# Kernel tuning notes

Hardware: AMD Instinct MI355X
Metric: run time of the kernel (lower is better)

The kernel has to match this reference:

```python
import jax, jax.numpy as jnp
import numpy as np

EMBED = 1024
HID = 1024
B, T = 32, 512


def _gru_layer(x, Wih, Whh, bih, bhh):
    """Torch-convention GRU over time. x: [B,T,Hin]; Wih: [3H,Hin]; Whh: [3H,H].
    Gate order (torch): reset, update, new."""
    H = Whh.shape[1]
    # Precompute input contributions for all timesteps: [T,B,3H]
    xg = jnp.einsum('bti,gi->tbg', x, Wih) + bih

    def step(h, xt):
        hg = h @ Whh.T + bhh                    # [B,3H]
        xr, xz, xn = jnp.split(xt, 3, axis=-1)
        hr, hz, hn = jnp.split(hg, 3, axis=-1)
        r = jax.nn.sigmoid(xr + hr)
        z = jax.nn.sigmoid(xz + hz)
        n = jnp.tanh(xn + r * hn)
        h_new = (1.0 - z) * n + z * h
        return h_new, h_new

    h0 = jnp.zeros((x.shape[0], H), dtype=x.dtype)
    _, ys = jax.lax.scan(step, h0, xg)          # ys: [T,B,H]
    return jnp.transpose(ys, (1, 0, 2))         # [B,T,H]


def setup_inputs() -> dict:
    key = jax.random.key(0)
    ks = jax.random.split(key, 16)
    s_in = 1.0 / np.sqrt(EMBED)
    s_h = 1.0 / np.sqrt(HID)
    return {
        'x': jax.random.normal(ks[0], (B, T, EMBED), jnp.float32),
        'context': jax.random.normal(ks[1], (B, HID), jnp.float32),
        'W_in': jax.random.uniform(ks[2], (HID, EMBED), jnp.float32, -s_in, s_in),
        'b_in': jax.random.uniform(ks[3], (HID,), jnp.float32, -s_in, s_in),
        'Wih0': jax.random.uniform(ks[4], (3 * HID, HID), jnp.float32, -s_h, s_h),
        'Whh0': jax.random.uniform(ks[5], (3 * HID, HID), jnp.float32, -s_h, s_h),
        'bih0': jax.random.uniform(ks[6], (3 * HID,), jnp.float32, -s_h, s_h),
        'bhh0': jax.random.uniform(ks[7], (3 * HID,), jnp.float32, -s_h, s_h),
        'Wih1': jax.random.uniform(ks[8], (3 * HID, HID), jnp.float32, -s_h, s_h),
        'Whh1': jax.random.uniform(ks[9], (3 * HID, HID), jnp.float32, -s_h, s_h),
        'bih1': jax.random.uniform(ks[10], (3 * HID,), jnp.float32, -s_h, s_h),
        'bhh1': jax.random.uniform(ks[11], (3 * HID,), jnp.float32, -s_h, s_h),
        'W_out': jax.random.uniform(ks[12], (EMBED, HID), jnp.float32, -s_h, s_h),
        'b_out': jax.random.uniform(ks[13], (EMBED,), jnp.float32, -s_h, s_h),
        'W_gate': jax.random.uniform(ks[14], (HID, HID), jnp.float32, -s_h, s_h),
        'b_gate': jax.random.uniform(ks[15], (HID,), jnp.float32, -s_h, s_h),
    }


def reference(x, context, W_in, b_in, Wih0, Whh0, bih0, bhh0,
              Wih1, Whh1, bih1, bhh1, W_out, b_out, W_gate, b_gate):
    # context_seq: [B,1,H] broadcast over time
    ctx = context[:, None, :]
    mixed = jnp.tanh(jnp.einsum('bte,he->bth', x, W_in) + b_in + ctx)
    h1 = _gru_layer(mixed, Wih0, Whh0, bih0, bhh0)
    h2 = _gru_layer(h1, Wih1, Whh1, bih1, bhh1)
    gate = jax.nn.sigmoid(jnp.einsum('bh,gh->bg', context, W_gate) + b_gate)
    gated = gate[:, None, :] * h2 + h2
    return jnp.einsum('bth,eh->bte', gated, W_out) + b_out
```

## Files before the change

### kernel.cpp

```cpp
#include <hip/hip_runtime.h>
#include <cstdint>
#include <cstddef>

#define SEQT  512
#define HID   1024
#define G3    3072
#define HSTR  1080
#define RING  32
#define FSTR  32

typedef __attribute__((ext_vector_type(8))) short bf16x8;
typedef __attribute__((ext_vector_type(8))) unsigned short u16x8;
typedef __attribute__((ext_vector_type(4))) float f32x4;

__device__ __forceinline__ float sigm(float x){ return 1.0f/(1.0f+expf(-x)); }
__device__ __forceinline__ float b2f(unsigned short s){ return __uint_as_float(((uint32_t)s)<<16); }
__device__ __forceinline__ unsigned short f2b(float f){
    uint32_t u=__float_as_uint(f);
    return (unsigned short)((u + 0x7FFFu + ((u>>16)&1u))>>16);
}

template<int ASRC, int BSRC, int MODE>
__global__ __launch_bounds__(256) void mfma_gemm(
    const void* __restrict__ Av, const void* __restrict__ Bv,
    const float* __restrict__ bias, const float* __restrict__ ctx,
    const float* __restrict__ gate, void* __restrict__ Cv,
    int N, int K)
{
    __shared__ __align__(16) unsigned short As[128*64];
    __shared__ __align__(16) unsigned short Bs[128*64];
    const int tid = threadIdx.x;
    const int lane = tid & 63;
    const int w = tid >> 6;
    const int wm = w & 1, wn = w >> 1;
    const int m0 = blockIdx.y * 128, n0 = blockIdx.x * 128;

    f32x4 acc[4][4];
#pragma unroll
    for (int i = 0; i < 4; i++)
#pragma unroll
        for (int j = 0; j < 4; j++) acc[i][j] = (f32x4){0.f,0.f,0.f,0.f};

    for (int kt = 0; kt < K; kt += 64) {
        __syncthreads();
        if (ASRC == 1) {
            const float* Af = (const float*)Av;
#pragma unroll
            for (int p = 0; p < 4; p++) {
                const int q = p*256 + tid, row = q>>3, kc = q&7;
                const float* src = Af + (size_t)(m0+row)*K + kt + kc*8;
                float4 u = *(const float4*)src, v = *(const float4*)(src+4);
                __align__(16) unsigned short tmp[8] =
                    {f2b(u.x),f2b(u.y),f2b(u.z),f2b(u.w),f2b(v.x),f2b(v.y),f2b(v.z),f2b(v.w)};
                *(bf16x8*)&As[row*64 + kc*8] = *(const bf16x8*)tmp;
            }
        } else {
            const unsigned short* Ab = (const unsigned short*)Av;
#pragma unroll
            for (int p = 0; p < 4; p++) {
                const int q = p*256 + tid, row = q>>3, kc = q&7;
                const int b = (m0+row) >> 9;
                u16x8 hv = *(const u16x8*)(Ab + (size_t)(m0+row)*K + kt + kc*8);
                const float* gp = gate + (size_t)b*HID + kt + kc*8;
                float4 g0 = *(const float4*)gp, g1 = *(const float4*)(gp+4);
                const float gg[8] = {g0.x,g0.y,g0.z,g0.w,g1.x,g1.y,g1.z,g1.w};
                __align__(16) unsigned short tmp[8];
#pragma unroll
                for (int e = 0; e < 8; e++)
                    tmp[e] = f2b(b2f(hv[e]) * (1.0f + gg[e]));
                *(bf16x8*)&As[row*64 + kc*8] = *(const bf16x8*)tmp;
            }
        }
        {
            const float* Bf = (const float*)Bv;
#pragma unroll
            for (int p = 0; p < 4; p++) {
                const int q = p*256 + tid, row = q>>3, kc = q&7;
                const float* src = Bf + (size_t)(n0+row)*K + kt + kc*8;
                float4 u = *(const float4*)src, v = *(const float4*)(src+4);
                __align__(16) unsigned short tmp[8] =
                    {f2b(u.x),f2b(u.y),f2b(u.z),f2b(u.w),f2b(v.x),f2b(v.y),f2b(v.z),f2b(v.w)};
                *(bf16x8*)&Bs[row*64 + kc*8] = *(const bf16x8*)tmp;
            }
        }
        __syncthreads();
#pragma unroll
        for (int kg = 0; kg < 2; kg++) {
            bf16x8 af[4], bfr[4];
#pragma unroll
            for (int mi = 0; mi < 4; mi++)
                af[mi] = *(const bf16x8*)&As[(wm*64+mi*16+(lane&15))*64 + kg*32 + (lane>>4)*8];
#pragma unroll
            for (int ni = 0; ni < 4; ni++)
                bfr[ni] = *(const bf16x8*)&Bs[(wn*64+ni*16+(lane&15))*64 + kg*32 + (lane>>4)*8];
#pragma unroll
            for (int mi = 0; mi < 4; mi++)
#pragma unroll
                for (int ni = 0; ni < 4; ni++)
                    acc[mi][ni] = __builtin_amdgcn_mfma_f32_16x16x32_bf16(
                        af[mi], bfr[ni], acc[mi][ni], 0, 0, 0);
        }
    }

    const int cl = lane & 15, rg = lane >> 4;
    const int bct = m0 >> 9;
#pragma unroll
    for (int mi = 0; mi < 4; mi++) {
        const int rowb = m0 + wm*64 + mi*16 + rg*4;
#pragma unroll
        for (int ni = 0; ni < 4; ni++) {
            const int col = n0 + wn*64 + ni*16 + cl;
            const float bv = bias[col];
            const float cv = (MODE==1) ? ctx[(size_t)bct*HID + col] : 0.0f;
#pragma unroll
            for (int r = 0; r < 4; r++) {
                float val = acc[mi][ni][r] + bv;
                if (MODE==1) val = tanhf(val + cv);
                const size_t off = (size_t)(rowb+r)*N + col;
                if (MODE==0) ((float*)Cv)[off] = val;
                else ((unsigned short*)Cv)[off] = f2b(val);
            }
        }
    }
}

__global__ __launch_bounds__(256) void gate_kernel(
    const float* __restrict__ ctx, const float* __restrict__ Wg,
    const float* __restrict__ bg, float* __restrict__ gate)
{
    const int j = blockIdx.x * 256 + threadIdx.x;
    const int b = blockIdx.y;
    const float4* cp = (const float4*)(ctx + (size_t)b * HID);
    const float4* wp = (const float4*)(Wg + (size_t)j * HID);
    float acc = 0.0f;
#pragma unroll 4
    for (int k = 0; k < HID / 4; k++) {
        float4 c = cp[k], w = wp[k];
        acc += c.x * w.x + c.y * w.y + c.z * w.z + c.w * w.w;
    }
    gate[(size_t)b * HID + j] = sigm(acc + bg[j]);
}

__device__ __forceinline__ void poll_ge(const unsigned int* p, unsigned int tgt)
{
    while (__hip_atomic_load(p, __ATOMIC_RELAXED, __HIP_MEMORY_SCOPE_AGENT) < tgt)
        __builtin_amdgcn_s_sleep(2);
}

__global__ __launch_bounds__(384, 1) void gru_pipe(
    const float* __restrict__ Wih0, const float* __restrict__ Whh0,
    const float* __restrict__ bih0, const float* __restrict__ bhh0,
    const float* __restrict__ Wih1, const float* __restrict__ Whh1,
    const float* __restrict__ bih1, const float* __restrict__ bhh1,
    const unsigned short* __restrict__ mixed,
    unsigned short* __restrict__ h1,
    unsigned short* __restrict__ h2,
    unsigned short* __restrict__ xgs0,
    unsigned short* __restrict__ xgs1,
    unsigned int* __restrict__ flags)
{
    __shared__ __align__(16) unsigned short h_lds[32*HSTR];
    __shared__ float sc[3][32][17];
    const int tid = threadIdx.x;
    const int lane = tid & 63;
    const int w = tid >> 6;
    const int bid = blockIdx.x;
    const int role = bid >> 6, rb = bid & 63;
    const int j0 = rb * 16;
    const int mh = w & 1, g = w >> 1;
    const int cl = lane & 15, kq = lane >> 4;

    unsigned int* fset[4] = { flags, flags + 64*FSTR, flags + 128*FSTR, flags + 192*FSTR };

    const float* Wsrc = (role == 0) ? Wih0 : (role == 1) ? Whh0
                      : (role == 2) ? Wih1 : Whh1;
    bf16x8 wreg[32];
    {
        const float* wr = Wsrc + (size_t)(g*1024 + j0 + cl)*1024 + kq*8;
#pragma unroll
        for (int kg = 0; kg < 32; kg++) {
            float4 u = *(const float4*)(wr + (size_t)kg*32);
            float4 v = *(const float4*)(wr + (size_t)kg*32 + 4);
            __align__(16) unsigned short tmp[8] =
                {f2b(u.x),f2b(u.y),f2b(u.z),f2b(u.w),f2b(v.x),f2b(v.y),f2b(v.z),f2b(v.w)};
            wreg[kg] = *(const bf16x8*)tmp;
        }
    }
#pragma unroll
    for (int kg = 0; kg < 32; kg++)
        asm volatile("" : "+v"(wreg[kg]));

    const int hrow_r = mh*16 + cl;
    const unsigned short* habase =
        &h_lds[hrow_r*HSTR + ((hrow_r & 3) << 4) + kq*8];

    auto stage = [&](const unsigned short* src_base, int tt) {
        for (int c = w; c < 64; c += 6) {
            const int r = c >> 1, hf = c & 1;
            const unsigned short* src =
                src_base + ((size_t)r*SEQT + tt)*HID + hf*512 + lane*8;
            __builtin_amdgcn_global_load_lds(
                (const __attribute__((address_space(1))) void*)src,
                (__attribute__((address_space(3))) void*)
                    &h_lds[r*HSTR + ((r & 3) << 4) + hf*512],
                16, 0, 0);
        }
    };

    if ((role & 1) == 0) {
        const unsigned short* hsrc = (role == 0) ? mixed : h1;
        unsigned short* xgs = ((role == 0) ? xgs0 : xgs1) + (size_t)rb*RING*32*48;
        const unsigned int* waitin = (role == 2) ? fset[1] : nullptr;
        const unsigned int* bp     = (role == 0) ? fset[1] : fset[3];
        unsigned int* myflag = &fset[role][rb*FSTR];

        for (int t = 0; t < SEQT; t++) {
            if (w == 0 && waitin)
                poll_ge(&waitin[lane*FSTR], (unsigned)(t+1));
            if (w == 1 && t >= RING && (t & 7) == 0)
                poll_ge(&bp[lane*FSTR], (unsigned)(t - 24));
            __syncthreads();

            stage(hsrc, t);
            asm volatile("s_waitcnt vmcnt(0)" ::: "memory");
            __syncthreads();

            f32x4 A[4];
#pragma unroll
            for (int i = 0; i < 4; i++) A[i] = (f32x4){0.f,0.f,0.f,0.f};
#pragma unroll
            for (int kg = 0; kg < 32; kg++) {
                bf16x8 hv = *(const bf16x8*)(habase + kg*32);
                A[kg & 3] = __builtin_amdgcn_mfma_f32_16x16x32_bf16(
                    hv, wreg[kg], A[kg & 3], 0, 0, 0);
            }
            f32x4 av = (A[0] + A[1]) + (A[2] + A[3]);
#pragma unroll
            for (int r = 0; r < 4; r++)
                sc[g][mh*16 + kq*4 + r][cl] = av[r];
            __syncthreads();

            if (tid < 192) {
                const int b = tid / 6, c16 = (tid % 6) * 8;
                unsigned short v[8];
#pragma unroll
                for (int k = 0; k < 8; k++) {
                    const int col = c16 + k;
                    v[k] = f2b(sc[col >> 4][b][col & 15]);
                }
                const uint64_t lo = (uint64_t)v[0] | ((uint64_t)v[1]<<16)
                                  | ((uint64_t)v[2]<<32) | ((uint64_t)v[3]<<48);
                const uint64_t hi = (uint64_t)v[4] | ((uint64_t)v[5]<<16)
                                  | ((uint64_t)v[6]<<32) | ((uint64_t)v[7]<<48);
                uint64_t* dst = (uint64_t*)(xgs + (((size_t)(t & (RING-1))*32 + b)*48 + c16));
                __hip_atomic_store(dst,   lo, __ATOMIC_RELAXED, __HIP_MEMORY_SCOPE_AGENT);
                __hip_atomic_store(dst+1, hi, __ATOMIC_RELAXED, __HIP_MEMORY_SCOPE_AGENT);
            }
            asm volatile("s_waitcnt vmcnt(0)" ::: "memory");
            __syncthreads();
            if (tid == 0)
                __hip_atomic_store(myflag, (unsigned)(t+1),
                                   __ATOMIC_RELAXED, __HIP_MEMORY_SCOPE_AGENT);
        }
    } else {
        const unsigned short* xgs = ((role == 1) ? xgs0 : xgs1) + (size_t)rb*RING*32*48;
        unsigned short* hdst = (role == 1) ? h1 : h2;
        const float* bih = (role == 1) ? bih0 : bih1;
        const float* bhh = (role == 1) ? bhh0 : bhh1;
        const unsigned int* peers = fset[role];
        const unsigned int* prodf = &fset[role-1][rb*FSTR];
        unsigned int* myflag = &fset[role][rb*FSTR];

        const int fb = tid >> 3;
        const int fj = (tid & 7) * 2;
        float hp0 = 0.f, hp1 = 0.f;
        float br0=0,br1=0,bz0=0,bz1=0,bni0=0,bni1=0,bnh0=0,bnh1=0;
        if (tid < 256) {
            br0 = bih[j0+fj]        + bhh[j0+fj];
            br1 = bih[j0+fj+1]      + bhh[j0+fj+1];
            bz0 = bih[HID+j0+fj]    + bhh[HID+j0+fj];
            bz1 = bih[HID+j0+fj+1]  + bhh[HID+j0+fj+1];
            bni0 = bih[2*HID+j0+fj];   bni1 = bih[2*HID+j0+fj+1];
            bnh0 = bhh[2*HID+j0+fj];   bnh1 = bhh[2*HID+j0+fj+1];
        }

        for (int t = 0; t < SEQT; t++) {
            if (w == 0 && t > 0)
                poll_ge(&peers[lane*FSTR], (unsigned)t);
            if (w == 2 && lane == 0)
                poll_ge(prodf, (unsigned)(t+1));
            __syncthreads();

            if (t > 0) stage(hdst, t-1);

            uint32_t xr2=0, xz2=0, xn2=0;
            if (tid < 256) {
                const unsigned short* xp = xgs + ((size_t)(t & (RING-1))*32 + fb)*48;
                xr2 = __hip_atomic_load((const unsigned int*)(xp + fj),
                                        __ATOMIC_RELAXED, __HIP_MEMORY_SCOPE_AGENT);
                xz2 = __hip_atomic_load((const unsigned int*)(xp + 16 + fj),
                                        __ATOMIC_RELAXED, __HIP_MEMORY_SCOPE_AGENT);
                xn2 = __hip_atomic_load((const unsigned int*)(xp + 32 + fj),
                                        __ATOMIC_RELAXED, __HIP_MEMORY_SCOPE_AGENT);
            }
            asm volatile("s_waitcnt vmcnt(0)" ::: "memory");
            __syncthreads();

            f32x4 A[4];
#pragma unroll
            for (int i = 0; i < 4; i++) A[i] = (f32x4){0.f,0.f,0.f,0.f};
            if (t > 0) {
#pragma unroll
                for (int kg = 0; kg < 32; kg++) {
                    bf16x8 hv = *(const bf16x8*)(habase + kg*32);
                    A[kg & 3] = __builtin_amdgcn_mfma_f32_16x16x32_bf16(
                        hv, wreg[kg], A[kg & 3], 0, 0, 0);
                }
            }
            f32x4 av = (A[0] + A[1]) + (A[2] + A[3]);
#pragma unroll
            for (int r = 0; r < 4; r++)
                sc[g][mh*16 + kq*4 + r][cl] = av[r];
            __syncthreads();

            if (tid < 256) {
                const float r0 = sigm(b2f((unsigned short)(xr2 & 0xFFFF)) + sc[0][fb][fj]   + br0);
                const float r1 = sigm(b2f((unsigned short)(xr2 >> 16))    + sc[0][fb][fj+1] + br1);
                const float z0 = sigm(b2f((unsigned short)(xz2 & 0xFFFF)) + sc[1][fb][fj]   + bz0);
                const float z1 = sigm(b2f((unsigned short)(xz2 >> 16))    + sc[1][fb][fj+1] + bz1);
                const float n0 = tanhf(b2f((unsigned short)(xn2 & 0xFFFF)) + bni0
                                       + r0*(sc[2][fb][fj]   + bnh0));
                const float n1 = tanhf(b2f((unsigned short)(xn2 >> 16))    + bni1
                                       + r1*(sc[2][fb][fj+1] + bnh1));
                const float h0 = (1.0f - z0)*n0 + z0*hp0;
                const float h1v = (1.0f - z1)*n1 + z1*hp1;
                hp0 = h0; hp1 = h1v;
                const uint32_t hv = (uint32_t)f2b(h0) | ((uint32_t)f2b(h1v) << 16);
                uint32_t* dst = (uint32_t*)(hdst + ((size_t)fb*SEQT + t)*HID + j0 + fj);
                __hip_atomic_store(dst, hv, __ATOMIC_RELAXED, __HIP_MEMORY_SCOPE_AGENT);
            }
            asm volatile("s_waitcnt vmcnt(0)" ::: "memory");
            __syncthreads();
            if (tid == 0)
                __hip_atomic_store(myflag, (unsigned)(t+1),
                                   __ATOMIC_RELAXED, __HIP_MEMORY_SCOPE_AGENT);
        }
    }
}

__global__ __launch_bounds__(256) void diag_kernel(float* __restrict__ out,
                                                   int n, float code)
{
    for (int i = blockIdx.x * 256 + threadIdx.x; i < n; i += gridDim.x * 256)
        out[i] = (i == 0) ? code : 0.0f;
}

extern "C" void kernel_launch(void* const* d_in, const int* in_sizes, int n_in,
                              void* d_out, int out_size, void* d_ws, size_t ws_size,
                              hipStream_t stream)
{
    const float* x      = (const float*)d_in[0];
    const float* ctx    = (const float*)d_in[1];
    const float* W_in   = (const float*)d_in[2];
    const float* b_in   = (const float*)d_in[3];
    const float* Wih0   = (const float*)d_in[4];
    const float* Whh0   = (const float*)d_in[5];
    const float* bih0   = (const float*)d_in[6];
    const float* bhh0   = (const float*)d_in[7];
    const float* Wih1   = (const float*)d_in[8];
    const float* Whh1   = (const float*)d_in[9];
    const float* bih1   = (const float*)d_in[10];
    const float* bhh1   = (const float*)d_in[11];
    const float* W_out  = (const float*)d_in[12];
    const float* b_out  = (const float*)d_in[13];
    const float* W_gate = (const float*)d_in[14];
    const float* b_gate = (const float*)d_in[15];
    float* out = (float*)d_out;

    const size_t MX = (size_t)16384 * 1024 * 2;
    const size_t XS = (size_t)64 * RING * 32 * 48 * 2;
    const size_t GT = (size_t)32 * 1024 * 4;
    const size_t FL = (size_t)4 * 64 * FSTR * 4;
    const size_t need = 3*MX + 2*XS + GT + FL;

    if (ws_size < need) {
        diag_kernel<<<2048, 256, 0, stream>>>(out, out_size, (float)(ws_size >> 20));
        return;
    }

    char* ws = (char*)d_ws;
    unsigned short* mixed = (unsigned short*)ws;
    unsigned short* h1    = (unsigned short*)(ws + MX);
    unsigned short* h2    = (unsigned short*)(ws + 2*MX);
    unsigned short* xgs0  = (unsigned short*)(ws + 3*MX);
    unsigned short* xgs1  = (unsigned short*)(ws + 3*MX + XS);
    float*          gate  = (float*)(ws + 3*MX + 2*XS);
    unsigned int*   flags = (unsigned int*)(ws + 3*MX + 2*XS + GT);

    hipMemsetAsync(flags, 0, FL, stream);
    gate_kernel<<<dim3(4, 32), 256, 0, stream>>>(ctx, W_gate, b_gate, gate);

    mfma_gemm<1, 1, 1><<<dim3(8, 128), 256, 0, stream>>>(
        x, W_in, b_in, ctx, nullptr, mixed, 1024, 1024);

    gru_pipe<<<256, 384, 0, stream>>>(
        Wih0, Whh0, bih0, bhh0, Wih1, Whh1, bih1, bhh1,
        mixed, h1, h2, xgs0, xgs1, flags);

    mfma_gemm<2, 1, 0><<<dim3(8, 128), 256, 0, stream>>>(
        h2, W_out, b_out, nullptr, gate, out, 1024, 1024);
}
```

Baseline: 2.390 ms.

## Split recurrent GRU step into two batch halves with split-K MFMA overlap

```diff
diff --git a/kernel.cpp b/kernel.cpp
--- a/kernel.cpp
+++ b/kernel.cpp
@@ -160,59 +160,45 @@
     unsigned int* __restrict__ flags)
 {
     __shared__ __align__(16) unsigned short h_lds[32*HSTR];
-    __shared__ float sc[3][32][17];
+    __shared__ float sc[1632];
     const int tid = threadIdx.x;
     const int lane = tid & 63;
     const int w = tid >> 6;
     const int bid = blockIdx.x;
     const int role = bid >> 6, rb = bid & 63;
     const int j0 = rb * 16;
-    const int mh = w & 1, g = w >> 1;
     const int cl = lane & 15, kq = lane >> 4;
 
-    unsigned int* fset[4] = { flags, flags + 64*FSTR, flags + 128*FSTR, flags + 192*FSTR };
-
-    const float* Wsrc = (role == 0) ? Wih0 : (role == 1) ? Whh0
-                      : (role == 2) ? Wih1 : Whh1;
-    bf16x8 wreg[32];
-    {
-        const float* wr = Wsrc + (size_t)(g*1024 + j0 + cl)*1024 + kq*8;
-#pragma unroll
-        for (int kg = 0; kg < 32; kg++) {
-            float4 u = *(const float4*)(wr + (size_t)kg*32);
-            float4 v = *(const float4*)(wr + (size_t)kg*32 + 4);
-            __align__(16) unsigned short tmp[8] =
-                {f2b(u.x),f2b(u.y),f2b(u.z),f2b(u.w),f2b(v.x),f2b(v.y),f2b(v.z),f2b(v.w)};
-            wreg[kg] = *(const bf16x8*)tmp;
-        }
-    }
-#pragma unroll
-    for (int kg = 0; kg < 32; kg++)
-        asm volatile("" : "+v"(wreg[kg]));
-
-    const int hrow_r = mh*16 + cl;
-    const unsigned short* habase =
-        &h_lds[hrow_r*HSTR + ((hrow_r & 3) << 4) + kq*8];
-
-    auto stage = [&](const unsigned short* src_base, int tt) {
-        for (int c = w; c < 64; c += 6) {
-            const int r = c >> 1, hf = c & 1;
-            const unsigned short* src =
-                src_base + ((size_t)r*SEQT + tt)*HID + hf*512 + lane*8;
-            __builtin_amdgcn_global_load_lds(
-                (const __attribute__((address_space(1))) void*)src,
-                (__attribute__((address_space(3))) void*)
-                    &h_lds[r*HSTR + ((r & 3) << 4) + hf*512],
-                16, 0, 0);
-        }
-    };
+    unsigned int* fset[6] = { flags,            flags + 64*FSTR,  flags + 128*FSTR,
+                              flags + 192*FSTR, flags + 256*FSTR, flags + 320*FSTR };
 
     if ((role & 1) == 0) {
+        const int g = w >> 1, mh = w & 1;
+        const float* Wsrc = (role == 0) ? Wih0 : Wih1;
+        bf16x8 wreg[32];
+        {
+            const float* wr = Wsrc + (size_t)(g*1024 + j0 + cl)*1024 + kq*8;
+#pragma unroll
+            for (int kg = 0; kg < 32; kg++) {
+                float4 u = *(const float4*)(wr + (size_t)kg*32);
+                float4 v = *(const float4*)(wr + (size_t)kg*32 + 4);
+                __align__(16) unsigned short tmp[8] =
+                    {f2b(u.x),f2b(u.y),f2b(u.z),f2b(u.w),f2b(v.x),f2b(v.y),f2b(v.z),f2b(v.w)};
+                wreg[kg] = *(const bf16x8*)tmp;
+            }
+        }
+#pragma unroll
+        for (int kg = 0; kg < 32; kg++) asm volatile("" : "+v"(wreg[kg]));
+
+        const int hrow_r = mh*16 + cl;
+        const unsigned short* habase =
+            &h_lds[hrow_r*HSTR + ((hrow_r & 3) << 4) + kq*8];
+
         const unsigned short* hsrc = (role == 0) ? mixed : h1;
         unsigned short* xgs = ((role == 0) ? xgs0 : xgs1) + (size_t)rb*RING*32*48;
-        const unsigned int* waitin = (role == 2) ? fset[1] : nullptr;
-        const unsigned int* bp     = (role == 0) ? fset[1] : fset[3];
-        unsigned int* myflag = &fset[role][rb*FSTR];
+        const unsigned int* waitin = (role == 2) ? fset[2] : nullptr;
+        const unsigned int* bp     = (role == 0) ? fset[2] : fset[5];
+        unsigned int* myflag = &fset[role == 0 ? 0 : 3][rb*FSTR];
 
         for (int t = 0; t < SEQT; t++) {
             if (w == 0 && waitin)
@@ -221,7 +207,16 @@
                 poll_ge(&bp[lane*FSTR], (unsigned)(t - 24));
             __syncthreads();
 
-            stage(hsrc, t);
+            for (int c = w; c < 64; c += 6) {
+                const int r = c >> 1, hf = c & 1;
+                const unsigned short* src =
+                    hsrc + ((size_t)r*SEQT + t)*HID + hf*512 + lane*8;
+                __builtin_amdgcn_global_load_lds(
+                    (const __attribute__((address_space(1))) void*)src,
+                    (__attribute__((address_space(3))) void*)
+                        &h_lds[r*HSTR + ((r & 3) << 4) + hf*512],
+                    16, 0, 0);
+            }
             asm volatile("s_waitcnt vmcnt(0)" ::: "memory");
             __syncthreads();
 
@@ -237,7 +232,7 @@
             f32x4 av = (A[0] + A[1]) + (A[2] + A[3]);
 #pragma unroll
             for (int r = 0; r < 4; r++)
-                sc[g][mh*16 + kq*4 + r][cl] = av[r];
+                sc[(g*32 + mh*16 + kq*4 + r)*17 + cl] = av[r];
             __syncthreads();
 
             if (tid < 192) {
@@ -246,7 +241,7 @@
 #pragma unroll
                 for (int k = 0; k < 8; k++) {
                     const int col = c16 + k;
-                    v[k] = f2b(sc[col >> 4][b][col & 15]);
+                    v[k] = f2b(sc[((col >> 4)*32 + b)*17 + (col & 15)]);
                 }
                 const uint64_t lo = (uint64_t)v[0] | ((uint64_t)v[1]<<16)
                                   | ((uint64_t)v[2]<<32) | ((uint64_t)v[3]<<48);
@@ -263,19 +258,43 @@
                                    __ATOMIC_RELAXED, __HIP_MEMORY_SCOPE_AGENT);
         }
     } else {
+        const int g = w >> 1, kh = w & 1;
+        const float* Wsrc = (role == 1) ? Whh0 : Whh1;
+        bf16x8 wreg[16];
+        {
+            const float* wr = Wsrc + (size_t)(g*1024 + j0 + cl)*1024 + kh*512 + kq*8;
+#pragma unroll
+            for (int kg = 0; kg < 16; kg++) {
+                float4 u = *(const float4*)(wr + (size_t)kg*32);
+                float4 v = *(const float4*)(wr + (size_t)kg*32 + 4);
+                __align__(16) unsigned short tmp[8] =
+                    {f2b(u.x),f2b(u.y),f2b(u.z),f2b(u.w),f2b(v.x),f2b(v.y),f2b(v.z),f2b(v.w)};
+                wreg[kg] = *(const bf16x8*)tmp;
+            }
+        }
+#pragma unroll
+        for (int kg = 0; kg < 16; kg++) asm volatile("" : "+v"(wreg[kg]));
+
+        unsigned short* hdst = (role == 1) ? h1 : h2;
         const unsigned short* xgs = ((role == 1) ? xgs0 : xgs1) + (size_t)rb*RING*32*48;
-        unsigned short* hdst = (role == 1) ? h1 : h2;
         const float* bih = (role == 1) ? bih0 : bih1;
         const float* bhh = (role == 1) ? bhh0 : bhh1;
-        const unsigned int* peers = fset[role];
-        const unsigned int* prodf = &fset[role-1][rb*FSTR];
-        unsigned int* myflag = &fset[role][rb*FSTR];
+        const unsigned int* prodf  = &fset[role == 1 ? 0 : 3][rb*FSTR];
+        unsigned int* setA = fset[role == 1 ? 1 : 4];
+        unsigned int* setB = fset[role == 1 ? 2 : 5];
+        unsigned int* myflagA = &setA[rb*FSTR];
+        unsigned int* myflagB = &setB[rb*FSTR];
+
+        const unsigned short* habaseA =
+            &h_lds[cl*HSTR + ((cl & 3) << 4) + kh*512 + kq*8];
+        const unsigned short* habaseB =
+            &h_lds[(16 + cl)*HSTR + ((cl & 3) << 4) + kh*512 + kq*8];
 
         const int fb = tid >> 3;
         const int fj = (tid & 7) * 2;
-        float hp0 = 0.f, hp1 = 0.f;
+        float hpA0=0.f, hpA1=0.f, hpB0=0.f, hpB1=0.f;
         float br0=0,br1=0,bz0=0,bz1=0,bni0=0,bni1=0,bnh0=0,bnh1=0;
-        if (tid < 256) {
+        if (tid < 128) {
             br0 = bih[j0+fj]        + bhh[j0+fj];
             br1 = bih[j0+fj+1]      + bhh[j0+fj+1];
             bz0 = bih[HID+j0+fj]    + bhh[HID+j0+fj];
@@ -286,16 +305,15 @@
 
         for (int t = 0; t < SEQT; t++) {
             if (w == 0 && t > 0)
-                poll_ge(&peers[lane*FSTR], (unsigned)t);
+                poll_ge(&setA[lane*FSTR], (unsigned)t);
             if (w == 2 && lane == 0)
                 poll_ge(prodf, (unsigned)(t+1));
             __syncthreads();
 
-            if (t > 0) stage(hdst, t-1);
-
             uint32_t xr2=0, xz2=0, xn2=0;
-            if (tid < 256) {
-                const unsigned short* xp = xgs + ((size_t)(t & (RING-1))*32 + fb)*48;
+            if (tid < 128) {
+                const unsigned short* xp =
+                    xgs + ((size_t)(t & (RING-1))*32 + fb)*48;
                 xr2 = __hip_atomic_load((const unsigned int*)(xp + fj),
                                         __ATOMIC_RELAXED, __HIP_MEMORY_SCOPE_AGENT);
                 xz2 = __hip_atomic_load((const unsigned int*)(xp + 16 + fj),
@@ -303,16 +321,31 @@
                 xn2 = __hip_atomic_load((const unsigned int*)(xp + 32 + fj),
                                         __ATOMIC_RELAXED, __HIP_MEMORY_SCOPE_AGENT);
             }
+            if (t > 0) {
+                for (int c = w; c < 32; c += 6) {
+                    const int r = c >> 1, hf = c & 1;
+                    const unsigned short* src =
+                        hdst + ((size_t)r*SEQT + (t-1))*HID + hf*512 + lane*8;
+                    __builtin_amdgcn_global_load_lds(
+                        (const __attribute__((address_space(1))) void*)src,
+                        (__attribute__((address_space(3))) void*)
+                            &h_lds[r*HSTR + ((r & 3) << 4) + hf*512],
+                        16, 0, 0);
+                }
+            }
             asm volatile("s_waitcnt vmcnt(0)" ::: "memory");
             __syncthreads();
+            if (tid == 0)
+                __hip_atomic_store(myflagB, (unsigned)t,
+                                   __ATOMIC_RELAXED, __HIP_MEMORY_SCOPE_AGENT);
 
             f32x4 A[4];
 #pragma unroll
             for (int i = 0; i < 4; i++) A[i] = (f32x4){0.f,0.f,0.f,0.f};
             if (t > 0) {
 #pragma unroll
-                for (int kg = 0; kg < 32; kg++) {
-                    bf16x8 hv = *(const bf16x8*)(habase + kg*32);
+                for (int kg = 0; kg < 16; kg++) {
+                    bf16x8 hv = *(const bf16x8*)(habaseA + kg*32);
                     A[kg & 3] = __builtin_amdgcn_mfma_f32_16x16x32_bf16(
                         hv, wreg[kg], A[kg & 3], 0, 0, 0);
                 }
@@ -320,31 +353,105 @@
             f32x4 av = (A[0] + A[1]) + (A[2] + A[3]);
 #pragma unroll
             for (int r = 0; r < 4; r++)
-                sc[g][mh*16 + kq*4 + r][cl] = av[r];
-            __syncthreads();
-
-            if (tid < 256) {
-                const float r0 = sigm(b2f((unsigned short)(xr2 & 0xFFFF)) + sc[0][fb][fj]   + br0);
-                const float r1 = sigm(b2f((unsigned short)(xr2 >> 16))    + sc[0][fb][fj+1] + br1);
-                const float z0 = sigm(b2f((unsigned short)(xz2 & 0xFFFF)) + sc[1][fb][fj]   + bz0);
-                const float z1 = sigm(b2f((unsigned short)(xz2 >> 16))    + sc[1][fb][fj+1] + bz1);
-                const float n0 = tanhf(b2f((unsigned short)(xn2 & 0xFFFF)) + bni0
-                                       + r0*(sc[2][fb][fj]   + bnh0));
-                const float n1 = tanhf(b2f((unsigned short)(xn2 >> 16))    + bni1
-                                       + r1*(sc[2][fb][fj+1] + bnh1));
-                const float h0 = (1.0f - z0)*n0 + z0*hp0;
-                const float h1v = (1.0f - z1)*n1 + z1*hp1;
-                hp0 = h0; hp1 = h1v;
+                sc[((g*2 + kh)*16 + kq*4 + r)*17 + cl] = av[r];
+            __syncthreads();
+
+            if (tid < 128) {
+                const float sr0 = sc[(0*16+fb)*17+fj]   + sc[(1*16+fb)*17+fj];
+                const float sr1 = sc[(0*16+fb)*17+fj+1] + sc[(1*16+fb)*17+fj+1];
+                const float sz0 = sc[(2*16+fb)*17+fj]   + sc[(3*16+fb)*17+fj];
+                const float sz1 = sc[(2*16+fb)*17+fj+1] + sc[(3*16+fb)*17+fj+1];
+                const float sn0 = sc[(4*16+fb)*17+fj]   + sc[(5*16+fb)*17+fj];
+                const float sn1 = sc[(4*16+fb)*17+fj+1] + sc[(5*16+fb)*17+fj+1];
+                const float r0 = sigm(b2f((unsigned short)(xr2 & 0xFFFF)) + sr0 + br0);
+                const float r1 = sigm(b2f((unsigned short)(xr2 >> 16))    + sr1 + br1);
+                const float z0 = sigm(b2f((unsigned short)(xz2 & 0xFFFF)) + sz0 + bz0);
+                const float z1 = sigm(b2f((unsigned short)(xz2 >> 16))    + sz1 + bz1);
+                const float n0 = tanhf(b2f((unsigned short)(xn2 & 0xFFFF)) + bni0 + r0*(sn0 + bnh0));
+                const float n1 = tanhf(b2f((unsigned short)(xn2 >> 16))    + bni1 + r1*(sn1 + bnh1));
+                const float h0 = (1.0f - z0)*n0 + z0*hpA0;
+                const float h1v = (1.0f - z1)*n1 + z1*hpA1;
+                hpA0 = h0; hpA1 = h1v;
                 const uint32_t hv = (uint32_t)f2b(h0) | ((uint32_t)f2b(h1v) << 16);
                 uint32_t* dst = (uint32_t*)(hdst + ((size_t)fb*SEQT + t)*HID + j0 + fj);
                 __hip_atomic_store(dst, hv, __ATOMIC_RELAXED, __HIP_MEMORY_SCOPE_AGENT);
             }
+
+            if (w == 0 && t > 0)
+                poll_ge(&setB[lane*FSTR], (unsigned)t);
+            __syncthreads();
+
+            if (tid < 128) {
+                const unsigned short* xp =
+                    xgs + ((size_t)(t & (RING-1))*32 + 16 + fb)*48;
+                xr2 = __hip_atomic_load((const unsigned int*)(xp + fj),
+                                        __ATOMIC_RELAXED, __HIP_MEMORY_SCOPE_AGENT);
+                xz2 = __hip_atomic_load((const unsigned int*)(xp + 16 + fj),
+                                        __ATOMIC_RELAXED, __HIP_MEMORY_SCOPE_AGENT);
+                xn2 = __hip_atomic_load((const unsigned int*)(xp + 32 + fj),
+                                        __ATOMIC_RELAXED, __HIP_MEMORY_SCOPE_AGENT);
+            }
+            if (t > 0) {
+                for (int c = w; c < 32; c += 6) {
+                    const int r = c >> 1, hf = c & 1;
+                    const int pr = 16 + r;
+                    const unsigned short* src =
+                        hdst + ((size_t)(16 + r)*SEQT + (t-1))*HID + hf*512 + lane*8;
+                    __builtin_amdgcn_global_load_lds(
+                        (const __attribute__((address_space(1))) void*)src,
+                        (__attribute__((address_space(3))) void*)
+                            &h_lds[pr*HSTR + ((pr & 3) << 4) + hf*512],
+                        16, 0, 0);
+                }
+            }
             asm volatile("s_waitcnt vmcnt(0)" ::: "memory");
             __syncthreads();
             if (tid == 0)
-                __hip_atomic_store(myflag, (unsigned)(t+1),
+                __hip_atomic_store(myflagA, (unsigned)(t+1),
                                    __ATOMIC_RELAXED, __HIP_MEMORY_SCOPE_AGENT);
-        }
+
+#pragma unroll
+            for (int i = 0; i < 4; i++) A[i] = (f32x4){0.f,0.f,0.f,0.f};
+            if (t > 0) {
+#pragma unroll
+                for (int kg = 0; kg < 16; kg++) {
+                    bf16x8 hv = *(const bf16x8*)(habaseB + kg*32);
+                    A[kg & 3] = __builtin_amdgcn_mfma_f32_16x16x32_bf16(
+                        hv, wreg[kg], A[kg & 3], 0, 0, 0);
+                }
+            }
+            av = (A[0] + A[1]) + (A[2] + A[3]);
+#pragma unroll
+            for (int r = 0; r < 4; r++)
+                sc[((g*2 + kh)*16 + kq*4 + r)*17 + cl] = av[r];
+            __syncthreads();
+
+            if (tid < 128) {
+                const float sr0 = sc[(0*16+fb)*17+fj]   + sc[(1*16+fb)*17+fj];
+                const float sr1 = sc[(0*16+fb)*17+fj+1] + sc[(1*16+fb)*17+fj+1];
+                const float sz0 = sc[(2*16+fb)*17+fj]   + sc[(3*16+fb)*17+fj];
+                const float sz1 = sc[(2*16+fb)*17+fj+1] + sc[(3*16+fb)*17+fj+1];
+                const float sn0 = sc[(4*16+fb)*17+fj]   + sc[(5*16+fb)*17+fj];
+                const float sn1 = sc[(4*16+fb)*17+fj+1] + sc[(5*16+fb)*17+fj+1];
+                const float r0 = sigm(b2f((unsigned short)(xr2 & 0xFFFF)) + sr0 + br0);
+                const float r1 = sigm(b2f((unsigned short)(xr2 >> 16))    + sr1 + br1);
+                const float z0 = sigm(b2f((unsigned short)(xz2 & 0xFFFF)) + sz0 + bz0);
+                const float z1 = sigm(b2f((unsigned short)(xz2 >> 16))    + sz1 + bz1);
+                const float n0 = tanhf(b2f((unsigned short)(xn2 & 0xFFFF)) + bni0 + r0*(sn0 + bnh0));
+                const float n1 = tanhf(b2f((unsigned short)(xn2 >> 16))    + bni1 + r1*(sn1 + bnh1));
+                const float h0 = (1.0f - z0)*n0 + z0*hpB0;
+                const float h1v = (1.0f - z1)*n1 + z1*hpB1;
+                hpB0 = h0; hpB1 = h1v;
+                const uint32_t hv = (uint32_t)f2b(h0) | ((uint32_t)f2b(h1v) << 16);
+                uint32_t* dst = (uint32_t*)(hdst + ((size_t)(16+fb)*SEQT + t)*HID + j0 + fj);
+                __hip_atomic_store(dst, hv, __ATOMIC_RELAXED, __HIP_MEMORY_SCOPE_AGENT);
+            }
+        }
+        asm volatile("s_waitcnt vmcnt(0)" ::: "memory");
+        __syncthreads();
+        if (tid == 0)
+            __hip_atomic_store(myflagB, (unsigned)SEQT,
+                               __ATOMIC_RELAXED, __HIP_MEMORY_SCOPE_AGENT);
     }
 }
 
@@ -380,7 +487,7 @@
     const size_t MX = (size_t)16384 * 1024 * 2;
     const size_t XS = (size_t)64 * RING * 32 * 48 * 2;
     const size_t GT = (size_t)32 * 1024 * 4;
-    const size_t FL = (size_t)4 * 64 * FSTR * 4;
+    const size_t FL = (size_t)6 * 64 * FSTR * 4;
     const size_t need = 3*MX + 2*XS + GT + FL;
 
     if (ws_size < need) {
```

Result: no change. 2.411 ms (+0.9%).

## Partition GRU pipeline by XCD with batch halves and XOR-swizzled LDS

Applied to the files above, without the earlier changes.

```diff
diff --git a/kernel.cpp b/kernel.cpp
--- a/kernel.cpp
+++ b/kernel.cpp
@@ -4,10 +4,10 @@
 
 #define SEQT  512
 #define HID   1024
-#define G3    3072
-#define HSTR  1080
+#define HSTR  1088
 #define RING  32
 #define FSTR  32
+#define RS    ((size_t)RING * 16 * 3072)
 
 typedef __attribute__((ext_vector_type(8))) short bf16x8;
 typedef __attribute__((ext_vector_type(8))) unsigned short u16x8;
@@ -155,189 +155,231 @@
     const unsigned short* __restrict__ mixed,
     unsigned short* __restrict__ h1,
     unsigned short* __restrict__ h2,
-    unsigned short* __restrict__ xgs0,
-    unsigned short* __restrict__ xgs1,
+    unsigned short* __restrict__ xgs,
     unsigned int* __restrict__ flags)
 {
-    __shared__ __align__(16) unsigned short h_lds[32*HSTR];
-    __shared__ float sc[3][32][17];
+    __shared__ __align__(16) unsigned short h_lds[40*HSTR];
+    __shared__ float sc[192*17];
+    __shared__ int s_xcd, s_rank;
+
     const int tid = threadIdx.x;
     const int lane = tid & 63;
     const int w = tid >> 6;
-    const int bid = blockIdx.x;
-    const int role = bid >> 6, rb = bid & 63;
-    const int j0 = rb * 16;
-    const int mh = w & 1, g = w >> 1;
     const int cl = lane & 15, kq = lane >> 4;
 
-    unsigned int* fset[4] = { flags, flags + 64*FSTR, flags + 128*FSTR, flags + 192*FSTR };
-
-    const float* Wsrc = (role == 0) ? Wih0 : (role == 1) ? Whh0
-                      : (role == 2) ? Wih1 : Whh1;
+    if (tid == 0) {
+        unsigned x;
+        asm volatile("s_getreg_b32 %0, hwreg(HW_REG_XCC_ID, 0, 32)" : "=s"(x));
+        x &= 7u;
+        s_xcd = (int)x;
+        s_rank = (int)atomicAdd(&flags[8*32*FSTR + x*16], 1u);
+    }
+    __syncthreads();
+    const int xcd = s_xcd;
+    const int rb  = s_rank & 31;
+    const int half = xcd & 1;
+    const int kind = xcd >> 1;
+    const int col0 = rb * 32;
+    const int bb   = half * 16;
+
+    unsigned int* fsetb = flags;
+
+    const int g = w >> 1, kh = w & 1;
+    const float* Wsrc = (kind==0) ? Whh0 : (kind==1) ? Wih1
+                      : (kind==2) ? Whh1 : Wih0;
     bf16x8 wreg[32];
-    {
-        const float* wr = Wsrc + (size_t)(g*1024 + j0 + cl)*1024 + kq*8;
-#pragma unroll
-        for (int kg = 0; kg < 32; kg++) {
+#pragma unroll
+    for (int nb = 0; nb < 2; nb++) {
+        const float* wr = Wsrc + (size_t)(g*1024 + col0 + nb*16 + cl)*1024 + kh*512 + kq*8;
+#pragma unroll
+        for (int kg = 0; kg < 16; kg++) {
             float4 u = *(const float4*)(wr + (size_t)kg*32);
             float4 v = *(const float4*)(wr + (size_t)kg*32 + 4);
             __align__(16) unsigned short tmp[8] =
                 {f2b(u.x),f2b(u.y),f2b(u.z),f2b(u.w),f2b(v.x),f2b(v.y),f2b(v.z),f2b(v.w)};
-            wreg[kg] = *(const bf16x8*)tmp;
-        }
-    }
-#pragma unroll
-    for (int kg = 0; kg < 32; kg++)
-        asm volatile("" : "+v"(wreg[kg]));
-
-    const int hrow_r = mh*16 + cl;
-    const unsigned short* habase =
-        &h_lds[hrow_r*HSTR + ((hrow_r & 3) << 4) + kq*8];
-
-    auto stage = [&](const unsigned short* src_base, int tt) {
-        for (int c = w; c < 64; c += 6) {
-            const int r = c >> 1, hf = c & 1;
-            const unsigned short* src =
-                src_base + ((size_t)r*SEQT + tt)*HID + hf*512 + lane*8;
-            __builtin_amdgcn_global_load_lds(
-                (const __attribute__((address_space(1))) void*)src,
-                (__attribute__((address_space(3))) void*)
-                    &h_lds[r*HSTR + ((r & 3) << 4) + hf*512],
-                16, 0, 0);
-        }
-    };
-
-    if ((role & 1) == 0) {
-        const unsigned short* hsrc = (role == 0) ? mixed : h1;
-        unsigned short* xgs = ((role == 0) ? xgs0 : xgs1) + (size_t)rb*RING*32*48;
-        const unsigned int* waitin = (role == 2) ? fset[1] : nullptr;
-        const unsigned int* bp     = (role == 0) ? fset[1] : fset[3];
-        unsigned int* myflag = &fset[role][rb*FSTR];
+            wreg[nb*16 + kg] = *(const bf16x8*)tmp;
+        }
+    }
+#pragma unroll
+    for (int i = 0; i < 32; i++) asm volatile("" : "+v"(wreg[i]));
+
+    const int rot = (cl & 7) << 4;
+    const char* hbytes = (const char*)h_lds;
+
+    unsigned short* ring = xgs + (size_t)((kind==0 || kind==3) ? half : 2+half) * RS;
+
+    if (kind == 0 || kind == 2) {
+        unsigned short* hdst = (kind == 0) ? h1 : h2;
+        const float* bih = (kind == 0) ? bih0 : bih1;
+        const float* bhh = (kind == 0) ? bhh0 : bhh1;
+        const unsigned int* peers = fsetb + xcd*32*FSTR;
+        const unsigned int* prod  = fsetb + ((kind==0) ? (6+half) : (2+half))*32*FSTR;
+        unsigned int* myflag = (unsigned int*)(peers + rb*FSTR);
+
+        const int fb = tid >> 4;
+        const int fj = (tid & 15) * 2;
+        float hp0 = 0.f, hp1 = 0.f;
+        float br0=0,br1=0,bz0=0,bz1=0,bni0=0,bni1=0,bnh0=0,bnh1=0;
+        if (tid < 256) {
+            const int jc = col0 + fj;
+            br0 = bih[jc]         + bhh[jc];
+            br1 = bih[jc+1]       + bhh[jc+1];
+            bz0 = bih[HID+jc]     + bhh[HID+jc];
+            bz1 = bih[HID+jc+1]   + bhh[HID+jc+1];
+            bni0 = bih[2*HID+jc];    bni1 = bih[2*HID+jc+1];
+            bnh0 = bhh[2*HID+jc];    bnh1 = bhh[2*HID+jc+1];
+        }
 
         for (int t = 0; t < SEQT; t++) {
-            if (w == 0 && waitin)
+            if (w == 0 && lane < 32 && t > 0)
+                poll_ge(&peers[lane*FSTR], (unsigned)t);
+            if (w == 2 && lane < 32 && (t & 7) == 0) {
+                const unsigned tgt = (t + 8 <= SEQT) ? (unsigned)(t + 8) : (unsigned)SEQT;
+                poll_ge(&prod[lane*FSTR], tgt);
+            }
+            __syncthreads();
+
+            uint32_t xr2=0, xz2=0, xn2=0;
+            if (tid < 256) {
+                const unsigned short* xp = ring + ((size_t)(t & (RING-1))*16 + fb)*3072;
+                xr2 = __hip_atomic_load((const unsigned int*)(xp + col0 + fj),
+                                        __ATOMIC_RELAXED, __HIP_MEMORY_SCOPE_AGENT);
+                xz2 = __hip_atomic_load((const unsigned int*)(xp + 1024 + col0 + fj),
+                                        __ATOMIC_RELAXED, __HIP_MEMORY_SCOPE_AGENT);
+                xn2 = __hip_atomic_load((const unsigned int*)(xp + 2048 + col0 + fj),
+                                        __ATOMIC_RELAXED, __HIP_MEMORY_SCOPE_AGENT);
+            }
+            if (t > 0) {
+                for (int c = w; c < 32; c += 6) {
+                    const int r = c >> 1, hf = c & 1;
+                    const char* src = (const char*)hdst
+                        + (((size_t)(bb + r)*SEQT + (t-1))*HID)*2
+                        + hf*1024 + ((lane*16) ^ ((r & 7) << 4));
+                    __builtin_amdgcn_global_load_lds(
+                        (const __attribute__((address_space(1))) void*)src,
+                        (__attribute__((address_space(3))) void*)
+                            ((char*)h_lds + r*2176 + hf*1024),
+                        16, 0, 0);
+                }
+            }
+            asm volatile("s_waitcnt vmcnt(0)" ::: "memory");
+            __syncthreads();
+
+            f32x4 A00={0.f,0.f,0.f,0.f}, A01=A00, A10=A00, A11=A00;
+            if (t > 0) {
+#pragma unroll
+                for (int kg = 0; kg < 16; kg++) {
+                    bf16x8 hv = *(const bf16x8*)(hbytes + cl*2176 +
+                        ((kh*1024 + kg*64 + kq*16) ^ rot));
+                    if (kg & 1) {
+                        A01 = __builtin_amdgcn_mfma_f32_16x16x32_bf16(hv, wreg[kg],    A01, 0,0,0);
+                        A11 = __builtin_amdgcn_mfma_f32_16x16x32_bf16(hv, wreg[16+kg], A11, 0,0,0);
+                    } else {
+                        A00 = __builtin_amdgcn_mfma_f32_16x16x32_bf16(hv, wreg[kg],    A00, 0,0,0);
+                        A10 = __builtin_amdgcn_mfma_f32_16x16x32_bf16(hv, wreg[16+kg], A10, 0,0,0);
+                    }
+                }
+            }
+            f32x4 av0 = A00 + A01, av1 = A10 + A11;
+#pragma unroll
+            for (int r = 0; r < 4; r++) {
+                sc[((g*4 + kh*2 + 0)*16 + kq*4 + r)*17 + cl] = av0[r];
+                sc[((g*4 + kh*2 + 1)*16 + kq*4 + r)*17 + cl] = av1[r];
+            }
+            __syncthreads();
+
+            if (tid < 256) {
+                const int c0 = fj, nb = c0 >> 4, cc = c0 & 15;
+                const float sr0 = sc[((0*4+nb)*16+fb)*17+cc]   + sc[((0*4+2+nb)*16+fb)*17+cc];
+                const float sr1 = sc[((0*4+nb)*16+fb)*17+cc+1] + sc[((0*4+2+nb)*16+fb)*17+cc+1];
+                const float sz0 = sc[((1*4+nb)*16+fb)*17+cc]   + sc[((1*4+2+nb)*16+fb)*17+cc];
+                const float sz1 = sc[((1*4+nb)*16+fb)*17+cc+1] + sc[((1*4+2+nb)*16+fb)*17+cc+1];
+                const float sn0 = sc[((2*4+nb)*16+fb)*17+cc]   + sc[((2*4+2+nb)*16+fb)*17+cc];
+                const float sn1 = sc[((2*4+nb)*16+fb)*17+cc+1] + sc[((2*4+2+nb)*16+fb)*17+cc+1];
+                const float r0 = sigm(b2f((unsigned short)(xr2 & 0xFFFF)) + sr0 + br0);
+                const float r1 = sigm(b2f((unsigned short)(xr2 >> 16))    + sr1 + br1);
+                const float z0 = sigm(b2f((unsigned short)(xz2 & 0xFFFF)) + sz0 + bz0);
+                const float z1 = sigm(b2f((unsigned short)(xz2 >> 16))    + sz1 + bz1);
+                const float n0 = tanhf(b2f((unsigned short)(xn2 & 0xFFFF)) + bni0 + r0*(sn0 + bnh0));
+                const float n1 = tanhf(b2f((unsigned short)(xn2 >> 16))    + bni1 + r1*(sn1 + bnh1));
+                const float h0 = (1.0f - z0)*n0 + z0*hp0;
+                const float h1v = (1.0f - z1)*n1 + z1*hp1;
+                hp0 = h0; hp1 = h1v;
+                const uint32_t hv = (uint32_t)f2b(h0) | ((uint32_t)f2b(h1v) << 16);
+                uint32_t* dst = (uint32_t*)(hdst + ((size_t)(bb+fb)*SEQT + t)*HID + col0 + fj);
+                __hip_atomic_store(dst, hv, __ATOMIC_RELAXED, __HIP_MEMORY_SCOPE_AGENT);
+            }
+            asm volatile("s_waitcnt vmcnt(0)" ::: "memory");
+            __syncthreads();
+            if (tid == 0)
+                __hip_atomic_store(myflag, (unsigned)(t+1),
+                                   __ATOMIC_RELAXED, __HIP_MEMORY_SCOPE_AGENT);
+        }
+    } else {
+        const unsigned short* src_base = (kind == 3) ? mixed : h1;
+        const unsigned int* waitin = (kind == 1) ? (fsetb + (0+half)*32*FSTR) : nullptr;
+        const unsigned int* bp = fsetb + ((kind==3) ? (0+half) : (4+half))*32*FSTR;
+        unsigned int* myflag = fsetb + xcd*32*FSTR + rb*FSTR;
+
+        for (int t = 0; t < SEQT; t++) {
+            if (w == 0 && lane < 32 && waitin)
                 poll_ge(&waitin[lane*FSTR], (unsigned)(t+1));
-            if (w == 1 && t >= RING && (t & 7) == 0)
+            if (w == 1 && lane < 32 && t >= RING && (t & 7) == 0)
                 poll_ge(&bp[lane*FSTR], (unsigned)(t - 24));
             __syncthreads();
 
-            stage(hsrc, t);
+            for (int c = w; c < 32; c += 6) {
+                const int r = c >> 1, hf = c & 1;
+                const char* src = (const char*)src_base
+                    + (((size_t)(bb + r)*SEQT + t)*HID)*2
+                    + hf*1024 + ((lane*16) ^ ((r & 7) << 4));
+                __builtin_amdgcn_global_load_lds(
+                    (const __attribute__((address_space(1))) void*)src,
+                    (__attribute__((address_space(3))) void*)
+                        ((char*)h_lds + r*2176 + hf*1024),
+                    16, 0, 0);
+            }
             asm volatile("s_waitcnt vmcnt(0)" ::: "memory");
             __syncthreads();
 
-            f32x4 A[4];
-#pragma unroll
-            for (int i = 0; i < 4; i++) A[i] = (f32x4){0.f,0.f,0.f,0.f};
-#pragma unroll
-            for (int kg = 0; kg < 32; kg++) {
-                bf16x8 hv = *(const bf16x8*)(habase + kg*32);
-                A[kg & 3] = __builtin_amdgcn_mfma_f32_16x16x32_bf16(
-                    hv, wreg[kg], A[kg & 3], 0, 0, 0);
-            }
-            f32x4 av = (A[0] + A[1]) + (A[2] + A[3]);
-#pragma unroll
-            for (int r = 0; r < 4; r++)
-                sc[g][mh*16 + kq*4 + r][cl] = av[r];
+            f32x4 A00={0.f,0.f,0.f,0.f}, A01=A00, A10=A00, A11=A00;
+#pragma unroll
+            for (int kg = 0; kg < 16; kg++) {
+                bf16x8 hv = *(const bf16x8*)(hbytes + cl*2176 +
+                    ((kh*1024 + kg*64 + kq*16) ^ rot));
+                if (kg & 1) {
+                    A01 = __builtin_amdgcn_mfma_f32_16x16x32_bf16(hv, wreg[kg],    A01, 0,0,0);
+                    A11 = __builtin_amdgcn_mfma_f32_16x16x32_bf16(hv, wreg[16+kg], A11, 0,0,0);
+                } else {
+                    A00 = __builtin_amdgcn_mfma_f32_16x16x32_bf16(hv, wreg[kg],    A00, 0,0,0);
+                    A10 = __builtin_amdgcn_mfma_f32_16x16x32_bf16(hv, wreg[16+kg], A10, 0,0,0);
+                }
+            }
+            f32x4 av0 = A00 + A01, av1 = A10 + A11;
+#pragma unroll
+            for (int r = 0; r < 4; r++) {
+                sc[((g*4 + kh*2 + 0)*16 + kq*4 + r)*17 + cl] = av0[r];
+                sc[((g*4 + kh*2 + 1)*16 + kq*4 + r)*17 + cl] = av1[r];
+            }
             __syncthreads();
 
             if (tid < 192) {
-                const int b = tid / 6, c16 = (tid % 6) * 8;
+                const int fb = tid / 12, gi = tid % 12;
+                const int gg = gi >> 2, c8 = (gi & 3) * 8;
                 unsigned short v[8];
 #pragma unroll
                 for (int k = 0; k < 8; k++) {
-                    const int col = c16 + k;
-                    v[k] = f2b(sc[col >> 4][b][col & 15]);
+                    const int c = c8 + k, nb = c >> 4, cc = c & 15;
+                    v[k] = f2b(sc[((gg*4+nb)*16+fb)*17+cc] + sc[((gg*4+2+nb)*16+fb)*17+cc]);
                 }
                 const uint64_t lo = (uint64_t)v[0] | ((uint64_t)v[1]<<16)
                                   | ((uint64_t)v[2]<<32) | ((uint64_t)v[3]<<48);
                 const uint64_t hi = (uint64_t)v[4] | ((uint64_t)v[5]<<16)
                                   | ((uint64_t)v[6]<<32) | ((uint64_t)v[7]<<48);
-                uint64_t* dst = (uint64_t*)(xgs + (((size_t)(t & (RING-1))*32 + b)*48 + c16));
+                uint64_t* dst = (uint64_t*)(ring + ((size_t)(t & (RING-1))*16 + fb)*3072
+                                            + gg*1024 + col0 + c8);
                 __hip_atomic_store(dst,   lo, __ATOMIC_RELAXED, __HIP_MEMORY_SCOPE_AGENT);
                 __hip_atomic_store(dst+1, hi, __ATOMIC_RELAXED, __HIP_MEMORY_SCOPE_AGENT);
-            }
-            asm volatile("s_waitcnt vmcnt(0)" ::: "memory");
-            __syncthreads();
-            if (tid == 0)
-                __hip_atomic_store(myflag, (unsigned)(t+1),
-                                   __ATOMIC_RELAXED, __HIP_MEMORY_SCOPE_AGENT);
-        }
-    } else {
-        const unsigned short* xgs = ((role == 1) ? xgs0 : xgs1) + (size_t)rb*RING*32*48;
-        unsigned short* hdst = (role == 1) ? h1 : h2;
-        const float* bih = (role == 1) ? bih0 : bih1;
-        const float* bhh = (role == 1) ? bhh0 : bhh1;
-        const unsigned int* peers = fset[role];
-        const unsigned int* prodf = &fset[role-1][rb*FSTR];
-        unsigned int* myflag = &fset[role][rb*FSTR];
-
-        const int fb = tid >> 3;
-        const int fj = (tid & 7) * 2;
-        float hp0 = 0.f, hp1 = 0.f;
-        float br0=0,br1=0,bz0=0,bz1=0,bni0=0,bni1=0,bnh0=0,bnh1=0;
-        if (tid < 256) {
-            br0 = bih[j0+fj]        + bhh[j0+fj];
-            br1 = bih[j0+fj+1]      + bhh[j0+fj+1];
-            bz0 = bih[HID+j0+fj]    + bhh[HID+j0+fj];
-            bz1 = bih[HID+j0+fj+1]  + bhh[HID+j0+fj+1];
-            bni0 = bih[2*HID+j0+fj];   bni1 = bih[2*HID+j0+fj+1];
-            bnh0 = bhh[2*HID+j0+fj];   bnh1 = bhh[2*HID+j0+fj+1];
-        }
-
-        for (int t = 0; t < SEQT; t++) {
-            if (w == 0 && t > 0)
-                poll_ge(&peers[lane*FSTR], (unsigned)t);
-            if (w == 2 && lane == 0)
-                poll_ge(prodf, (unsigned)(t+1));
-            __syncthreads();
-
-            if (t > 0) stage(hdst, t-1);
-
-            uint32_t xr2=0, xz2=0, xn2=0;
-            if (tid < 256) {
-                const unsigned short* xp = xgs + ((size_t)(t & (RING-1))*32 + fb)*48;
-                xr2 = __hip_atomic_load((const unsigned int*)(xp + fj),
-                                        __ATOMIC_RELAXED, __HIP_MEMORY_SCOPE_AGENT);
-                xz2 = __hip_atomic_load((const unsigned int*)(xp + 16 + fj),
-                                        __ATOMIC_RELAXED, __HIP_MEMORY_SCOPE_AGENT);
-                xn2 = __hip_atomic_load((const unsigned int*)(xp + 32 + fj),
-                                        __ATOMIC_RELAXED, __HIP_MEMORY_SCOPE_AGENT);
-            }
-            asm volatile("s_waitcnt vmcnt(0)" ::: "memory");
-            __syncthreads();
-
-            f32x4 A[4];
-#pragma unroll
-            for (int i = 0; i < 4; i++) A[i] = (f32x4){0.f,0.f,0.f,0.f};
-            if (t > 0) {
-#pragma unroll
-                for (int kg = 0; kg < 32; kg++) {
-                    bf16x8 hv = *(const bf16x8*)(habase + kg*32);
-                    A[kg & 3] = __builtin_amdgcn_mfma_f32_16x16x32_bf16(
-                        hv, wreg[kg], A[kg & 3], 0, 0, 0);
-                }
-            }
-            f32x4 av = (A[0] + A[1]) + (A[2] + A[3]);
-#pragma unroll
-            for (int r = 0; r < 4; r++)
-                sc[g][mh*16 + kq*4 + r][cl] = av[r];
-            __syncthreads();
-
-            if (tid < 256) {
-                const float r0 = sigm(b2f((unsigned short)(xr2 & 0xFFFF)) + sc[0][fb][fj]   + br0);
-                const float r1 = sigm(b2f((unsigned short)(xr2 >> 16))    + sc[0][fb][fj+1] + br1);
-                const float z0 = sigm(b2f((unsigned short)(xz2 & 0xFFFF)) + sc[1][fb][fj]   + bz0);
-                const float z1 = sigm(b2f((unsigned short)(xz2 >> 16))    + sc[1][fb][fj+1] + bz1);
-                const float n0 = tanhf(b2f((unsigned short)(xn2 & 0xFFFF)) + bni0
-                                       + r0*(sc[2][fb][fj]   + bnh0));
-                const float n1 = tanhf(b2f((unsigned short)(xn2 >> 16))    + bni1
-                                       + r1*(sc[2][fb][fj+1] + bnh1));
-                const float h0 = (1.0f - z0)*n0 + z0*hp0;
-                const float h1v = (1.0f - z1)*n1 + z1*hp1;
-                hp0 = h0; hp1 = h1v;
-                const uint32_t hv = (uint32_t)f2b(h0) | ((uint32_t)f2b(h1v) << 16);
-                uint32_t* dst = (uint32_t*)(hdst + ((size_t)fb*SEQT + t)*HID + j0 + fj);
-                __hip_atomic_store(dst, hv, __ATOMIC_RELAXED, __HIP_MEMORY_SCOPE_AGENT);
             }
             asm volatile("s_waitcnt vmcnt(0)" ::: "memory");
             __syncthreads();
@@ -377,11 +419,11 @@
     const float* b_gate = (const float*)d_in[15];
     float* out = (float*)d_out;
 
-    const size_t MX = (size_t)16384 * 1024 * 2;
-    const size_t XS = (size_t)64 * RING * 32 * 48 * 2;
-    const size_t GT = (size_t)32 * 1024 * 4;
-    const size_t FL = (size_t)4 * 64 * FSTR * 4;
-    const size_t need = 3*MX + 2*XS + GT + FL;
+    const size_t MX  = (size_t)16384 * 1024 * 2;
+    const size_t XGS = (size_t)4 * RS * 2;
+    const size_t GT  = (size_t)32 * 1024 * 4;
+    const size_t FL  = (size_t)(8*32*FSTR + 256) * 4;
+    const size_t need = 3*MX + XGS + GT + FL;
 
     if (ws_size < need) {
         diag_kernel<<<2048, 256, 0, stream>>>(out, out_size, (float)(ws_size >> 20));
@@ -392,10 +434,9 @@
     unsigned short* mixed = (unsigned short*)ws;
     unsigned short* h1    = (unsigned short*)(ws + MX);
     unsigned short* h2    = (unsigned short*)(ws + 2*MX);
-    unsigned short* xgs0  = (unsigned short*)(ws + 3*MX);
-    unsigned short* xgs1  = (unsigned short*)(ws + 3*MX + XS);
-    float*          gate  = (float*)(ws + 3*MX + 2*XS);
-    unsigned int*   flags = (unsigned int*)(ws + 3*MX + 2*XS + GT);
+    unsigned short* xgs   = (unsigned short*)(ws + 3*MX);
+    float*          gate  = (float*)(ws + 3*MX + XGS);
+    unsigned int*   flags = (unsigned int*)(ws + 3*MX + XGS + GT);
 
     hipMemsetAsync(flags, 0, FL, stream);
     gate_kernel<<<dim3(4, 32), 256, 0, stream>>>(ctx, W_gate, b_gate, gate);
@@ -405,7 +446,7 @@
 
     gru_pipe<<<256, 384, 0, stream>>>(
         Wih0, Whh0, bih0, bhh0, Wih1, Whh1, bih1, bhh1,
-        mixed, h1, h2, xgs0, xgs1, flags);
+        mixed, h1, h2, xgs, flags);
 
     mfma_gemm<2, 1, 0><<<dim3(8, 128), 256, 0, stream>>>(
         h2, W_out, b_out, nullptr, gate, out, 1024, 1024);
```

After: 2.103 ms. 12.0% less time.
